# Kernel tuning notes

Hardware: AMD Instinct MI355X
Metric: run time of the kernel (lower is better)

## Reference

```python
import jax, jax.numpy as jnp
import numpy as np

N_NODES = 10000
N_EDGES = 320000
D_IN = 256
D_HID = 256
N_CLASSES = 40


def _init_linear(key, fan_in, fan_out):
    kw, kb = jax.random.split(key)
    bound = 1.0 / np.sqrt(fan_in)
    W = jax.random.uniform(kw, (fan_in, fan_out), jnp.float32, -bound, bound)
    b = jax.random.uniform(kb, (fan_out,), jnp.float32, -bound, bound)
    return W, b


def setup_inputs() -> dict:
    key = jax.random.key(0)
    k0, k1, k2, k3, k4 = jax.random.split(key, 5)
    node_features = jax.random.normal(k0, (N_NODES, D_IN), jnp.float32)
    edge_index = jax.random.randint(k1, (2, N_EDGES), 0, N_NODES, jnp.int64)
    W1, b1 = _init_linear(k2, D_IN, D_HID)
    W2, b2 = _init_linear(k3, D_HID, D_HID)
    W3, b3 = _init_linear(k4, D_HID, N_CLASSES)
    return {"node_features": node_features, "edge_index": edge_index,
            "W1": W1, "b1": b1, "W2": W2, "b2": b2, "W3": W3, "b3": b3}


def _mp_layer(x, src, dst, W, b):
    # message: linear transform of source-node features (transform-then-gather
    # is mathematically identical to gather-then-transform and cheaper when E>N)
    msg = (x @ W + b)[src]                      # [E, d_out]
    # scatter sum-aggregate messages at destination nodes
    out = jax.ops.segment_sum(msg, dst, num_segments=N_NODES)  # [N, d_out]
    return out


def reference(node_features, edge_index, W1, b1, W2, b2, W3, b3):
    src, dst = edge_index[0], edge_index[1]
    x = jax.nn.relu(_mp_layer(node_features, src, dst, W1, b1))
    x = jax.nn.relu(_mp_layer(x, src, dst, W2, b2))
    x = jax.nn.relu(_mp_layer(x, src, dst, W3, b3))
    return x
```

## Files before the change

kernel.cpp:

```cpp
#include <hip/hip_runtime.h>


#define N_NODES   10000
#define N_EDGES   320000
#define D_HID     256
#define N_CLASSES 40
#define CAP       96

typedef __attribute__((ext_vector_type(8))) short short8;
typedef __attribute__((ext_vector_type(4))) float f32x4;

__device__ __forceinline__ ushort f2bf(float f) {
    unsigned u = __float_as_uint(f);
    u = (u + 0x7fffu + ((u >> 16) & 1u)) >> 16;
    return (ushort)u;
}
__device__ __forceinline__ float bf2f(ushort u) {
    return __uint_as_float(((unsigned)u) << 16);
}


__global__ __launch_bounds__(256)
void prep_kernel(const float* __restrict__ X,
                 const float* __restrict__ W1, const float* __restrict__ W2,
                 const float* __restrict__ W3,
                 ushort* __restrict__ Xb, ushort* __restrict__ bufY,
                 ushort* __restrict__ bufH,
                 ushort* __restrict__ W1b, ushort* __restrict__ W2b,
                 ushort* __restrict__ W3b, int* __restrict__ cursor,
                 int* __restrict__ esrc) {
    const int tid  = blockIdx.x * 256 + threadIdx.x;
    const int nthr = gridDim.x * 256;
    for (int i = tid; i < N_NODES; i += nthr) cursor[i] = 0;
    for (int i = tid; i < N_NODES * CAP; i += nthr) esrc[i] = N_NODES;
    ushort4 z; z.x = 0; z.y = 0; z.z = 0; z.w = 0;
    if (tid < 64) {
        ((ushort4*)Xb)[640000 + tid]   = z;
        ((ushort4*)bufY)[640000 + tid] = z;
    }
    if (tid < 10) ((ushort4*)bufH)[100000 + tid] = z;
    for (int i = tid; i < N_NODES * D_HID / 4; i += nthr) {
        float4 v = ((const float4*)X)[i];
        ushort4 o;
        o.x = f2bf(v.x); o.y = f2bf(v.y); o.z = f2bf(v.z); o.w = f2bf(v.w);
        ((ushort4*)Xb)[i] = o;
    }
    for (int i = tid; i < 141312; i += nthr) {
        if (i < 65536) {
            int n = i >> 8, k = i & 255;
            W1b[i] = f2bf(W1[k * 256 + n]);
        } else if (i < 131072) {
            int t2 = i - 65536;
            int n = t2 >> 8, k = t2 & 255;
            W2b[t2] = f2bf(W2[k * 256 + n]);
        } else {
            int t2 = i - 131072;
            int n = t2 >> 8, k = t2 & 255;
            W3b[t2] = f2bf(W3[k * N_CLASSES + n]);
        }
    }
}


__global__ __launch_bounds__(256)
void place_kernel(const int* __restrict__ edges, int* __restrict__ cursor,
                  int* __restrict__ esrc) {
    int e = blockIdx.x * 256 + threadIdx.x;
    if (e < N_EDGES) {
        int d = edges[N_EDGES + e];
        int pos = atomicAdd(&cursor[d], 1);
        if (pos < CAP) esrc[d * CAP + pos] = edges[e];
    }
}


#define LDSA 264

template<bool CHAIN>
__global__ __launch_bounds__(256)
void layer_kernel(const ushort* __restrict__ Xin, const ushort* __restrict__ Bt,
                  const float* __restrict__ bias,
                  const int* __restrict__ deg, const int* __restrict__ esrc,
                  const ushort* __restrict__ W3b, const float* __restrict__ b3,
                  ushort* __restrict__ Out) {
    __shared__ ushort As[16 * LDSA];
    __shared__ ushort Bs[40 * LDSA];
    __shared__ int    eidxL[16 * CAP];
    __shared__ int    degI[16];
    __shared__ float  degF[16];

    const int tid = threadIdx.x;
    const int wave = tid >> 6, lane = tid & 63;
    const int lr = lane & 15, lg = lane >> 4;
    const int rowBase = blockIdx.x * 16;

#pragma unroll
    for (int p = 0; p < 6; ++p) {
        int idx = p * 256 + tid;
        eidxL[idx] = esrc[rowBase * CAP + idx];
    }
    if (tid < 16) {
        int c = deg[rowBase + tid];
        degF[tid] = (float)c;
        degI[tid] = (c > CAP) ? CAP : c;
    }
    __syncthreads();

    const uint2* hp = (const uint2*)Xin;
#pragma unroll 1
    for (int it = 0; it < 4; ++it) {
        int nl = wave * 4 + it;
        int cntp = (degI[nl] + 7) & ~7;
        float a0 = 0.f, a1 = 0.f, a2 = 0.f, a3 = 0.f;
#pragma unroll 1
        for (int i = 0; i < cntp; i += 8) {
            uint2 v[8];
#pragma unroll
            for (int u = 0; u < 8; ++u) {
                int s = eidxL[nl * CAP + i + u];
                v[u] = hp[(size_t)s * 64 + lane];
            }
#pragma unroll
            for (int u = 0; u < 8; ++u) {
                a0 += bf2f((ushort)(v[u].x & 0xffff));
                a1 += bf2f((ushort)(v[u].x >> 16));
                a2 += bf2f((ushort)(v[u].y & 0xffff));
                a3 += bf2f((ushort)(v[u].y >> 16));
            }
        }
        uint2 o;
        o.x = (unsigned)f2bf(a0) | ((unsigned)f2bf(a1) << 16);
        o.y = (unsigned)f2bf(a2) | ((unsigned)f2bf(a3) << 16);
        *(uint2*)(As + nl * LDSA + lane * 4) = o;
    }

    f32x4 acc[4] = {};
    for (int k0 = 0; k0 < 256; k0 += 32) {
        __syncthreads();
#pragma unroll
        for (int p = 0; p < 4; ++p) {
            int idx = p * 256 + tid;
            int n = idx >> 2, c = (idx & 3) * 8;
            *(uint4*)(Bs + n * 40 + c) = *(const uint4*)(Bt + (size_t)n * 256 + k0 + c);
        }
        __syncthreads();
        short8 af = *(const short8*)(As + lr * LDSA + k0 + lg * 8);
#pragma unroll
        for (int j = 0; j < 4; ++j) {
            short8 bf = *(const short8*)(Bs + (wave * 64 + j * 16 + lr) * 40 + lg * 8);
            acc[j] = __builtin_amdgcn_mfma_f32_16x16x32_bf16(af, bf, acc[j], 0, 0, 0);
        }
    }

    if (!CHAIN) {
#pragma unroll
        for (int j = 0; j < 4; ++j) {
            int col = wave * 64 + j * 16 + lr;
            float bv = bias[col];
#pragma unroll
            for (int r = 0; r < 4; ++r) {
                int grow = rowBase + lg * 4 + r;
                float dg = degF[lg * 4 + r];
                Out[(size_t)grow * 256 + col] = f2bf(fmaxf(fmaf(dg, bv, acc[j][r]), 0.f));
            }
        }
    } else {
        __syncthreads();
#pragma unroll
        for (int j = 0; j < 4; ++j) {
            int col = wave * 64 + j * 16 + lr;
            float bv = bias[col];
#pragma unroll
            for (int r = 0; r < 4; ++r) {
                int rl = lg * 4 + r;
                As[rl * LDSA + col] = f2bf(fmaxf(fmaf(degF[rl], bv, acc[j][r]), 0.f));
            }
        }
#pragma unroll
        for (int p = 0; p < 5; ++p) {
            int idx = p * 256 + tid;
            int n = idx >> 5, c = (idx & 31) * 8;
            *(uint4*)(Bs + n * LDSA + c) = *(const uint4*)(W3b + (size_t)n * 256 + c);
        }
        __syncthreads();
        if (wave < 3) {
            f32x4 acc3 = {};
            for (int k0 = 0; k0 < 256; k0 += 32) {
                short8 af = *(const short8*)(As + lr * LDSA + k0 + lg * 8);
                short8 bf = *(const short8*)(Bs + (wave * 16 + lr) * LDSA + k0 + lg * 8);
                acc3 = __builtin_amdgcn_mfma_f32_16x16x32_bf16(af, bf, acc3, 0, 0, 0);
            }
            int col = wave * 16 + lr;
            if (col < N_CLASSES) {
                float bv = b3[col];
#pragma unroll
                for (int r = 0; r < 4; ++r) {
                    int grow = rowBase + lg * 4 + r;
                    Out[(size_t)grow * N_CLASSES + col] = f2bf(acc3[r] + bv);
                }
            }
        }
    }
}


__global__ __launch_bounds__(256)
void agg_relu_40_kernel(const ushort* __restrict__ h, const int* __restrict__ deg,
                        const int* __restrict__ esrc, float* __restrict__ out) {
    int wv   = threadIdx.x >> 6;
    int lane = threadIdx.x & 63;
    int node = (blockIdx.x << 2) + wv;
    if (node >= N_NODES) return;
    int cnt = deg[node];
    if (cnt > CAP) cnt = CAP;
    int cntp = (cnt + 7) & ~7;
    const int* ep = esrc + node * CAP;
    if (lane < N_CLASSES) {
        float a = 0.f, b = 0.f;
#pragma unroll 1
        for (int i = 0; i < cntp; i += 8) {
            int s[8];
#pragma unroll
            for (int u = 0; u < 8; ++u) s[u] = ep[i + u];
#pragma unroll
            for (int u = 0; u < 8; u += 2) {
                a += bf2f(h[(size_t)s[u]     * N_CLASSES + lane]);
                b += bf2f(h[(size_t)s[u + 1] * N_CLASSES + lane]);
            }
        }
        out[(size_t)node * N_CLASSES + lane] = fmaxf(a + b, 0.f);
    }
}


extern "C" void kernel_launch(void* const* d_in, const int* in_sizes, int n_in,
                              void* d_out, int out_size, void* d_ws, size_t ws_size,
                              hipStream_t stream) {
    const float* X     = (const float*)d_in[0];
    const int*   edges = (const int*)d_in[1];
    const float* W1 = (const float*)d_in[2];
    const float* b1 = (const float*)d_in[3];
    const float* W2 = (const float*)d_in[4];
    const float* b2 = (const float*)d_in[5];
    const float* W3 = (const float*)d_in[6];
    const float* b3 = (const float*)d_in[7];
    float* out = (float*)d_out;

    char* ws = (char*)d_ws;
    ushort* Xb   = (ushort*)(ws);
    ushort* bufY = (ushort*)(ws + 5120512);
    ushort* bufH = (ushort*)(ws + 10241024);
    ushort* W1b  = (ushort*)(ws + 11041104);
    ushort* W2b  = (ushort*)(ws + 11172176);
    ushort* W3b  = (ushort*)(ws + 11303248);
    int*   cursor = (int*)(ws + 11323728);
    int*   esrc   = (int*)(ws + 11363728);

    prep_kernel<<<512, 256, 0, stream>>>(X, W1, W2, W3, Xb, bufY, bufH,
                                         W1b, W2b, W3b, cursor, esrc);
    place_kernel<<<(N_EDGES + 255) / 256, 256, 0, stream>>>(edges, cursor, esrc);
    layer_kernel<false><<<N_NODES / 16, 256, 0, stream>>>(
        Xb, W1b, b1, cursor, esrc, W3b, b3, bufY);
    layer_kernel<true><<<N_NODES / 16, 256, 0, stream>>>(
        bufY, W2b, b2, cursor, esrc, W3b, b3, bufH);
    agg_relu_40_kernel<<<(N_NODES + 3) / 4, 256, 0, stream>>>(bufH, cursor, esrc, out);
}
```

Before: 159.4 us.

## Double-buffer gathers across nodes, prefetch weights into registers, vectorize final aggregation

The layer kernel's gather loop is replaced by a software-pipelined stream. It uses 16-byte loads where each half-wave handles alternate edges, and register double-buffering lets loads for the next chunk issue while the current chunk is accumulated, even across node boundaries. Weight tiles for the GEMM are prefetched into registers one k-step ahead so global latency overlaps the MFMA work. The 40-class aggregation kernel now uses 8-byte vector loads over 6 edge groups per wave, with shuffle reductions, and fully unrolls up to 96 edges. This raises register pressure and relies on the degree cap of 96.

```diff
diff --git a/kernel.cpp b/kernel.cpp
--- a/kernel.cpp
+++ b/kernel.cpp
@@ -92,6 +92,7 @@
     const int tid = threadIdx.x;
     const int wave = tid >> 6, lane = tid & 63;
     const int lr = lane & 15, lg = lane >> 4;
+    const int lo = lane & 31, hi = lane >> 5;
     const int rowBase = blockIdx.x * 16;
 
 #pragma unroll
@@ -106,32 +107,98 @@
     }
     __syncthreads();
 
-    const uint2* hp = (const uint2*)Xin;
+    uint4 wreg[4];
+    auto loadW = [&](int k0) {
+#pragma unroll
+        for (int p = 0; p < 4; ++p) {
+            int idx = p * 256 + tid;
+            int n = idx >> 2, c = (idx & 3) * 8;
+            wreg[p] = *(const uint4*)(Bt + (size_t)n * 256 + k0 + c);
+        }
+    };
+    loadW(0);
+
+    const uint4* hp4 = (const uint4*)Xin;
+
+    unsigned bpack = 0; int total = 0;
+#pragma unroll
+    for (int it = 0; it < 4; ++it) {
+        int nb = (degI[wave * 4 + it] + 15) >> 4;
+        bpack |= (unsigned)nb << (8 * it);
+        total += nb;
+    }
+#pragma unroll
+    for (int it = 0; it < 4; ++it) {
+        if (((bpack >> (8 * it)) & 255u) == 0u && lane < 32) {
+            uint4 z{};
+            *((uint4*)(As + (wave * 4 + it) * LDSA) + lane) = z;
+        }
+    }
+
+    int issIt = 0;
+    while (issIt < 4 && ((bpack >> (8 * issIt)) & 255u) == 0u) ++issIt;
+    int issRem = (issIt < 4) ? (int)((bpack >> (8 * issIt)) & 255u) : 0;
+    int issOff = 0;
+    int conIt = issIt, conRem = issRem;
+
+    uint4 vA[8], vB[8];
+    float a[8] = {};
+
+    auto ISSUE = [&](uint4* v) {
+        int ibase = (wave * 4 + issIt) * CAP + issOff;
+#pragma unroll
+        for (int u = 0; u < 8; ++u) {
+            int e = eidxL[ibase + 2 * u + hi];
+            v[u] = hp4[(size_t)e * 32 + lo];
+        }
+        issOff += 16;
+        if (--issRem == 0) {
+            do { ++issIt; } while (issIt < 4 && ((bpack >> (8 * issIt)) & 255u) == 0u);
+            issRem = (issIt < 4) ? (int)((bpack >> (8 * issIt)) & 255u) : 0;
+            issOff = 0;
+        }
+    };
+    auto FLUSH = [&]() {
+#pragma unroll
+        for (int j = 0; j < 8; ++j) a[j] += __shfl_xor(a[j], 32);
+        if (lane < 32) {
+            uint4 o;
+            o.x = (unsigned)f2bf(a[0]) | ((unsigned)f2bf(a[1]) << 16);
+            o.y = (unsigned)f2bf(a[2]) | ((unsigned)f2bf(a[3]) << 16);
+            o.z = (unsigned)f2bf(a[4]) | ((unsigned)f2bf(a[5]) << 16);
+            o.w = (unsigned)f2bf(a[6]) | ((unsigned)f2bf(a[7]) << 16);
+            *((uint4*)(As + (wave * 4 + conIt) * LDSA) + lane) = o;
+        }
+#pragma unroll
+        for (int j = 0; j < 8; ++j) a[j] = 0.f;
+    };
+    auto CONSUME = [&](uint4* v) {
+#pragma unroll
+        for (int u = 0; u < 8; ++u) {
+            a[0] += bf2f((ushort)(v[u].x & 0xffff)); a[1] += bf2f((ushort)(v[u].x >> 16));
+            a[2] += bf2f((ushort)(v[u].y & 0xffff)); a[3] += bf2f((ushort)(v[u].y >> 16));
+            a[4] += bf2f((ushort)(v[u].z & 0xffff)); a[5] += bf2f((ushort)(v[u].z >> 16));
+            a[6] += bf2f((ushort)(v[u].w & 0xffff)); a[7] += bf2f((ushort)(v[u].w >> 16));
+        }
+        if (--conRem == 0) {
+            FLUSH();
+            do { ++conIt; } while (conIt < 4 && ((bpack >> (8 * conIt)) & 255u) == 0u);
+            conRem = (conIt < 4) ? (int)((bpack >> (8 * conIt)) & 255u) : 0;
+        }
+    };
+
+    if (total > 0) {
+        ISSUE(vA);
+        int done = 0;
 #pragma unroll 1
-    for (int it = 0; it < 4; ++it) {
-        int nl = wave * 4 + it;
-        int cntp = (degI[nl] + 7) & ~7;
-        float a0 = 0.f, a1 = 0.f, a2 = 0.f, a3 = 0.f;
-#pragma unroll 1
-        for (int i = 0; i < cntp; i += 8) {
-            uint2 v[8];
-#pragma unroll
-            for (int u = 0; u < 8; ++u) {
-                int s = eidxL[nl * CAP + i + u];
-                v[u] = hp[(size_t)s * 64 + lane];
-            }
-#pragma unroll
-            for (int u = 0; u < 8; ++u) {
-                a0 += bf2f((ushort)(v[u].x & 0xffff));
-                a1 += bf2f((ushort)(v[u].x >> 16));
-                a2 += bf2f((ushort)(v[u].y & 0xffff));
-                a3 += bf2f((ushort)(v[u].y >> 16));
-            }
-        }
-        uint2 o;
-        o.x = (unsigned)f2bf(a0) | ((unsigned)f2bf(a1) << 16);
-        o.y = (unsigned)f2bf(a2) | ((unsigned)f2bf(a3) << 16);
-        *(uint2*)(As + nl * LDSA + lane * 4) = o;
+        while (true) {
+            if (done + 1 < total) ISSUE(vB);
+            CONSUME(vA);
+            if (++done >= total) break;
+            if (done + 1 < total) ISSUE(vA);
+            CONSUME(vB);
+            if (++done >= total) break;
+        }
     }
 
     f32x4 acc[4] = {};
@@ -141,9 +208,10 @@
         for (int p = 0; p < 4; ++p) {
             int idx = p * 256 + tid;
             int n = idx >> 2, c = (idx & 3) * 8;
-            *(uint4*)(Bs + n * 40 + c) = *(const uint4*)(Bt + (size_t)n * 256 + k0 + c);
+            *(uint4*)(Bs + n * 40 + c) = wreg[p];
         }
         __syncthreads();
+        if (k0 + 32 < 256) loadW(k0 + 32);
         short8 af = *(const short8*)(As + lr * LDSA + k0 + lg * 8);
 #pragma unroll
         for (int j = 0; j < 4; ++j) {
@@ -207,28 +275,59 @@
 __global__ __launch_bounds__(256)
 void agg_relu_40_kernel(const ushort* __restrict__ h, const int* __restrict__ deg,
                         const int* __restrict__ esrc, float* __restrict__ out) {
-    int wv   = threadIdx.x >> 6;
-    int lane = threadIdx.x & 63;
-    int node = (blockIdx.x << 2) + wv;
+    const int wv   = threadIdx.x >> 6;
+    const int lane = threadIdx.x & 63;
+    const int node = (blockIdx.x << 2) + wv;
     if (node >= N_NODES) return;
     int cnt = deg[node];
     if (cnt > CAP) cnt = CAP;
-    int cntp = (cnt + 7) & ~7;
     const int* ep = esrc + node * CAP;
-    if (lane < N_CLASSES) {
-        float a = 0.f, b = 0.f;
-#pragma unroll 1
-        for (int i = 0; i < cntp; i += 8) {
-            int s[8];
-#pragma unroll
-            for (int u = 0; u < 8; ++u) s[u] = ep[i + u];
-#pragma unroll
-            for (int u = 0; u < 8; u += 2) {
-                a += bf2f(h[(size_t)s[u]     * N_CLASSES + lane]);
-                b += bf2f(h[(size_t)s[u + 1] * N_CLASSES + lane]);
-            }
-        }
-        out[(size_t)node * N_CLASSES + lane] = fmaxf(a + b, 0.f);
+    const int l6  = (lane < 60) ? lane : 0;
+    const int g6  = l6 / 10;
+    const int c10 = l6 - g6 * 10;
+    const int nb  = (cnt + 47) / 48;
+
+    uint2 v0[8], v1[8];
+    if (nb > 0) {
+#pragma unroll
+        for (int u = 0; u < 8; ++u) {
+            int s = ep[6 * u + g6];
+            v0[u] = *(const uint2*)(h + (size_t)s * N_CLASSES + c10 * 4);
+        }
+    }
+    if (nb > 1) {
+#pragma unroll
+        for (int u = 0; u < 8; ++u) {
+            int s = ep[48 + 6 * u + g6];
+            v1[u] = *(const uint2*)(h + (size_t)s * N_CLASSES + c10 * 4);
+        }
+    }
+    float a0 = 0.f, a1 = 0.f, a2 = 0.f, a3 = 0.f;
+    if (nb > 0) {
+#pragma unroll
+        for (int u = 0; u < 8; ++u) {
+            a0 += bf2f((ushort)(v0[u].x & 0xffff)); a1 += bf2f((ushort)(v0[u].x >> 16));
+            a2 += bf2f((ushort)(v0[u].y & 0xffff)); a3 += bf2f((ushort)(v0[u].y >> 16));
+        }
+    }
+    if (nb > 1) {
+#pragma unroll
+        for (int u = 0; u < 8; ++u) {
+            a0 += bf2f((ushort)(v1[u].x & 0xffff)); a1 += bf2f((ushort)(v1[u].x >> 16));
+            a2 += bf2f((ushort)(v1[u].y & 0xffff)); a3 += bf2f((ushort)(v1[u].y >> 16));
+        }
+    }
+#define FOLD40(x) { x += __shfl(x, lane + 30);                      \
+                    float t1 = __shfl(x, lane + 10);                \
+                    float t2 = __shfl(x, lane + 20);                \
+                    x += t1 + t2; }
+    FOLD40(a0); FOLD40(a1); FOLD40(a2); FOLD40(a3);
+#undef FOLD40
+    if (lane < 10) {
+        float4 o;
+        o.x = fmaxf(a0, 0.f); o.y = fmaxf(a1, 0.f);
+        o.z = fmaxf(a2, 0.f); o.w = fmaxf(a3, 0.f);
+        *(float4*)(out + (size_t)node * N_CLASSES + lane * 4) = o;
     }
 }
 
```

Measured after the change: 211.7 us. 1.33x slower.
